# Performance work log

Measured on AMD Instinct MI355X. Metric: run time of the kernel, lower is better.

Reference implementation:

```python
import jax, jax.numpy as jnp
import numpy as np

N_NODES = 100000
N_EDGES = 1600000
HID = 128


def setup_inputs() -> dict:
    key = jax.random.key(0)
    ks = jax.random.split(key, 12)
    s = lambda fan_in: 1.0 / np.sqrt(fan_in)
    return {
        "x": jax.random.normal(ks[0], (N_NODES, HID), jnp.float32),
        "edge_index": jax.random.randint(ks[1], (2, N_EDGES), 0, N_NODES, jnp.int64),
        "edge_attr": jax.random.uniform(ks[2], (N_EDGES,), jnp.float32),
        "W_enc": jax.random.normal(ks[3], (HID, HID), jnp.float32) * s(HID),
        "b_enc": jax.random.normal(ks[4], (HID,), jnp.float32) * s(HID),
        "W_msg": jax.random.normal(ks[5], (HID + 1, HID), jnp.float32) * s(HID + 1),
        "b_msg": jax.random.normal(ks[6], (HID,), jnp.float32) * s(HID + 1),
        "W_upd": jax.random.normal(ks[7], (2 * HID, HID), jnp.float32) * s(2 * HID),
        "b_upd": jax.random.normal(ks[8], (HID,), jnp.float32) * s(2 * HID),
        "W_dec": jax.random.normal(ks[9], (HID, 1), jnp.float32) * s(HID),
        "b_dec": jax.random.normal(ks[10], (1,), jnp.float32) * s(HID),
    }


def reference(x, edge_index, edge_attr, W_enc, b_enc, W_msg, b_msg,
              W_upd, b_upd, W_dec, b_dec):
    n = x.shape[0]
    # encoder + relu
    h = jax.nn.relu(x @ W_enc + b_enc)                       # [N, H]
    src, dst = edge_index[0], edge_index[1]
    # message: gather x_j, concat scalar edge_attr, linear
    m = jnp.concatenate([h[src], edge_attr[:, None]], axis=-1) @ W_msg + b_msg  # [E, H]
    # scatter-min aggregate per destination node (nodes w/o in-edges -> 0, PyG convention)
    agg = jax.ops.segment_min(m, dst, num_segments=n)        # [N, H]
    agg = jnp.where(jnp.isinf(agg), jnp.zeros((), m.dtype), agg)
    # update: concat + linear
    u = jnp.concatenate([h, agg], axis=-1) @ W_upd + b_upd   # [N, H]
    # decoder + sigmoid
    return jax.nn.sigmoid(u @ W_dec + b_dec)                 # [N, 1]
```

## Files before the change

### kernel.cpp

```cpp
#include <hip/hip_runtime.h>

#define NN 100000
#define NE 1600000
#define HID 128
#define NBUCK 1563
#define CAP 1280
#define STP 130
#define SENT 3.0e38f
#define CH 8192
#define NCH 196
#define ENCB 391

typedef float f32x4 __attribute__((ext_vector_type(4)));
typedef __bf16 bf16x8 __attribute__((ext_vector_type(8)));
typedef unsigned short u16x8 __attribute__((ext_vector_type(8)));

static __device__ __forceinline__ unsigned short f2bf(float f) {
  union { float f; unsigned u; } v; v.f = f;
  unsigned u = v.u;
  return (unsigned short)((u + 0x7FFFu + ((u >> 16) & 1u)) >> 16);
}

static __device__ __forceinline__ f32x4 mfma_bf16(u16x8 a, u16x8 b, f32x4 c) {
  return __builtin_amdgcn_mfma_f32_16x16x32_bf16(
      __builtin_bit_cast(bf16x8, a), __builtin_bit_cast(bf16x8, b), c, 0, 0, 0);
}

static __device__ __forceinline__ int gidx(const int* __restrict__ ei, int is64, long long pos) {
  return is64 ? ei[pos * 2] : ei[pos];
}
static __device__ __forceinline__ int detect64(const int* __restrict__ ei, int tid) {
  unsigned long long bl = __ballot(ei[2 * (tid & 63) + 1] == 0);
  return (bl == ~0ull) ? 1 : 0;
}

__global__ __launch_bounds__(512) void k_prepw(const float* __restrict__ Wenc,
    const float* __restrict__ Wmsg, const float* __restrict__ Wupd,
    const float* __restrict__ Wdec, unsigned short* __restrict__ Wb,
    float* __restrict__ vprep, int* __restrict__ gcursor) {
  int b = blockIdx.x;
  int t = threadIdx.x;
  if (b == 96) {
    if (t < 128) {
      const float* row = Wupd + (size_t)(128 + t) * 128;
      float s = 0.f;
#pragma unroll 8
      for (int j = 0; j < 128; ++j) s = fmaf(row[j], Wdec[j], s);
      vprep[t] = s;
    }
    for (int i = t; i < NBUCK; i += 512) gcursor[i] = i * CAP;
    return;
  }
  int i = b * 512 + t;
  int m = i >> 14, idx = i & 16383;
  const float* src = (m == 0) ? Wenc : ((m == 1) ? Wmsg : Wupd);
  int k = idx >> 7, j = idx & 127;
  Wb[m * 17408 + j * 136 + k] = f2bf(src[idx]);
}

__global__ __launch_bounds__(512) void k_enc2(const float* __restrict__ x,
    const float* __restrict__ benc, const float* __restrict__ bupd,
    const float* __restrict__ Wdec, const unsigned short* __restrict__ Wb,
    unsigned* __restrict__ mNp, float* __restrict__ hdec) {
  __shared__ __align__(16) unsigned short Wt3[3 * 17408];
  __shared__ float bshE[128];
  __shared__ float bshU[128];
  __shared__ float wdsh[128];
  __shared__ unsigned short bounce[8][16 * 136];
  int tid = threadIdx.x;

  for (int i = tid; i < 6528; i += 512)
    ((uint4*)Wt3)[i] = ((const uint4*)Wb)[i];
  if (tid < 128) { bshE[tid] = benc[tid]; bshU[tid] = bupd[tid]; wdsh[tid] = Wdec[tid]; }
  __syncthreads();
  const unsigned short* WtE = Wt3;
  const unsigned short* WtM = Wt3 + 17408;
  const unsigned short* WtU = Wt3 + 2 * 17408;

  int wave = tid >> 6, lane = tid & 63;
  int l15 = lane & 15, lg = lane >> 4;
  f32x4 zero = {0.f, 0.f, 0.f, 0.f};

  for (int g = 0; g < 2; ++g) {
    int rowBase = blockIdx.x * 256 + g * 128 + wave * 16;
    int nodeA = rowBase + l15; if (nodeA > NN - 1) nodeA = NN - 1;

    u16x8 af[4];
#pragma unroll
    for (int kt = 0; kt < 4; ++kt) {
      const float* px = x + (long long)nodeA * HID + kt * 32 + lg * 8;
      f32x4 a0 = *(const f32x4*)px;
      f32x4 a1 = *(const f32x4*)(px + 4);
      u16x8 t;
      t[0] = f2bf(a0[0]); t[1] = f2bf(a0[1]); t[2] = f2bf(a0[2]); t[3] = f2bf(a0[3]);
      t[4] = f2bf(a1[0]); t[5] = f2bf(a1[1]); t[6] = f2bf(a1[2]); t[7] = f2bf(a1[3]);
      af[kt] = t;
    }
    f32x4 acc[8];
#pragma unroll
    for (int nt = 0; nt < 8; ++nt) acc[nt] = zero;
#pragma unroll
    for (int kt = 0; kt < 4; ++kt)
#pragma unroll
      for (int nt = 0; nt < 8; ++nt) {
        u16x8 bfv = *(const u16x8*)&WtE[(nt * 16 + l15) * 136 + kt * 32 + lg * 8];
        acc[nt] = mfma_bf16(af[kt], bfv, acc[nt]);
      }
#pragma unroll
    for (int nt = 0; nt < 8; ++nt) {
      int j = nt * 16 + l15;
      float bj = bshE[j];
#pragma unroll
      for (int r = 0; r < 4; ++r) {
        float v = acc[nt][r] + bj;
        v = v > 0.f ? v : 0.f;
        bounce[wave][(lg * 4 + r) * 136 + j] = f2bf(v);
      }
    }
    u16x8 ha[4];
#pragma unroll
    for (int kt = 0; kt < 4; ++kt)
      ha[kt] = *(const u16x8*)&bounce[wave][l15 * 136 + kt * 32 + lg * 8];
    asm volatile("s_waitcnt lgkmcnt(0)" ::: "memory");
    __builtin_amdgcn_sched_barrier(0);

    f32x4 acc2[8];
#pragma unroll
    for (int nt = 0; nt < 8; ++nt) acc2[nt] = zero;
#pragma unroll
    for (int kt = 0; kt < 4; ++kt)
#pragma unroll
      for (int nt = 0; nt < 8; ++nt) {
        u16x8 bfv = *(const u16x8*)&WtM[(nt * 16 + l15) * 136 + kt * 32 + lg * 8];
        acc2[nt] = mfma_bf16(ha[kt], bfv, acc2[nt]);
      }
#pragma unroll
    for (int nt = 0; nt < 8; ++nt) {
      int j = nt * 16 + l15;
#pragma unroll
      for (int r = 0; r < 4; ++r)
        bounce[wave][(lg * 4 + r) * 136 + j] = f2bf(acc2[nt][r]);
    }
    asm volatile("s_waitcnt lgkmcnt(0)" ::: "memory");
    __builtin_amdgcn_sched_barrier(0);
#pragma unroll 4
    for (int row = 0; row < 16; ++row) {
      int node = rowBase + row;
      if (node < NN) {
        unsigned lo = bounce[wave][row * 136 + lane];
        unsigned hi = bounce[wave][row * 136 + 64 + lane];
        mNp[(size_t)node * 64 + lane] = lo | (hi << 16);
      }
    }

    f32x4 acc3[8];
#pragma unroll
    for (int nt = 0; nt < 8; ++nt) acc3[nt] = zero;
#pragma unroll
    for (int kt = 0; kt < 4; ++kt)
#pragma unroll
      for (int nt = 0; nt < 8; ++nt) {
        u16x8 bfv = *(const u16x8*)&WtU[(nt * 16 + l15) * 136 + kt * 32 + lg * 8];
        acc3[nt] = mfma_bf16(ha[kt], bfv, acc3[nt]);
      }
    float hs0 = 0.f, hs1 = 0.f, hs2 = 0.f, hs3 = 0.f;
#pragma unroll
    for (int nt = 0; nt < 8; ++nt) {
      int j = nt * 16 + l15;
      float bu = bshU[j], wv = wdsh[j];
      hs0 += (acc3[nt][0] + bu) * wv;
      hs1 += (acc3[nt][1] + bu) * wv;
      hs2 += (acc3[nt][2] + bu) * wv;
      hs3 += (acc3[nt][3] + bu) * wv;
    }
#pragma unroll
    for (int m = 1; m < 16; m <<= 1) {
      hs0 += __shfl_xor(hs0, m);
      hs1 += __shfl_xor(hs1, m);
      hs2 += __shfl_xor(hs2, m);
      hs3 += __shfl_xor(hs3, m);
    }
    if (l15 == 0) {
      int n0 = rowBase + lg * 4;
      if (n0 + 3 < NN) {
        float4 st4; st4.x = hs0; st4.y = hs1; st4.z = hs2; st4.w = hs3;
        *(float4*)&hdec[n0] = st4;
      } else {
        if (n0 + 0 < NN) hdec[n0 + 0] = hs0;
        if (n0 + 1 < NN) hdec[n0 + 1] = hs1;
        if (n0 + 2 < NN) hdec[n0 + 2] = hs2;
        if (n0 + 3 < NN) hdec[n0 + 3] = hs3;
      }
    }
  }
}

__global__ __launch_bounds__(512) void k_sortscatter(const int* __restrict__ ei,
    const float* __restrict__ ea, int* __restrict__ gcursor,
    unsigned long long* __restrict__ csr) {
  __shared__ unsigned gbase[NBUCK];
  __shared__ unsigned cnt[NBUCK];
  int tid = threadIdx.x;
  int chunk = blockIdx.x;
  long long base = (long long)chunk * CH;
  int n = (int)(((long long)NE - base < CH) ? ((long long)NE - base) : CH);
  int is64 = detect64(ei, tid);
  for (int i = tid; i < NBUCK; i += 512) cnt[i] = 0;
  __syncthreads();
  for (int i = tid; i < n; i += 512) {
    int d = gidx(ei, is64, (long long)NE + base + i);
    atomicAdd(&cnt[d >> 6], 1u);
  }
  __syncthreads();
  for (int b = tid; b < NBUCK; b += 512) {
    unsigned c = cnt[b];
    gbase[b] = c ? (unsigned)atomicAdd(&gcursor[b], (int)c) : 0u;
  }
  __syncthreads();
  for (int i = tid; i < NBUCK; i += 512) cnt[i] = 0;
  __syncthreads();
  for (int i = tid; i < n; i += 512) {
    int s = gidx(ei, is64, base + i);
    int d = gidx(ei, is64, (long long)NE + base + i);
    unsigned eab = f2bf(ea[base + i]);
    int b = d >> 6;
    unsigned lp = atomicAdd(&cnt[b], 1u);
    unsigned lo = (unsigned)(s << 6) | ((unsigned)(d & 63) << 23);
    csr[gbase[b] + lp] = (unsigned long long)lo | ((unsigned long long)eab << 48);
  }
}

__global__ __launch_bounds__(512, 8) void k_msg(const unsigned* __restrict__ mNp,
    const float* __restrict__ Wmsg, const int* __restrict__ gcursor,
    const unsigned long long* __restrict__ csr, const float* __restrict__ bmsg,
    const float* __restrict__ vprep, const float* __restrict__ hdec,
    const float* __restrict__ bdec, float* __restrict__ out) {
  __shared__ float stf[64 * STP];
  int tid = threadIdx.x;
  int b = blockIdx.x;
  for (int i = tid; i < 64 * STP; i += 512) stf[i] = SENT;
  __syncthreads();

  int lane = tid & 63;
  int wv = tid >> 6;
  int off = b * CAP, end = gcursor[b];
  int cntE = end - off;
  int per = (cntE + 7) >> 3;
  int i0 = off + wv * per;
  int i1 = i0 + per; if (i1 > end) i1 = end;
  int iu = __builtin_amdgcn_readfirstlane(i0);
  int ie = __builtin_amdgcn_readfirstlane(i1);
  float wl0 = Wmsg[128 * 128 + lane];
  float wl1 = Wmsg[128 * 128 + 64 + lane];

#define EDGE_DO(PK, VV) do { \
    int loc_ = (int)(((unsigned)(PK) >> 23) & 0x3Fu); \
    float ea_ = __uint_as_float((unsigned)((PK) >> 32) & 0xFFFF0000u); \
    float a0_ = fmaf(ea_, wl0, __uint_as_float((VV) << 16)); \
    float a1_ = fmaf(ea_, wl1, __uint_as_float((VV) & 0xFFFF0000u)); \
    atomicMin(&stf[loc_ * STP + lane], a0_); \
    atomicMin(&stf[loc_ * STP + 64 + lane], a1_); \
  } while (0)

  int i = iu;
  for (; i + 16 <= ie; i += 16) {
    unsigned long long pk[16];
#pragma unroll
    for (int j = 0; j < 16; ++j) pk[j] = csr[i + j];
    unsigned v[16];
#pragma unroll
    for (int j = 0; j < 16; ++j)
      v[j] = mNp[((unsigned)pk[j] & 0x7FFFFFu) + lane];
#pragma unroll
    for (int j = 0; j < 16; ++j) EDGE_DO(pk[j], v[j]);
  }
  for (; i + 4 <= ie; i += 4) {
    unsigned long long pk[4];
#pragma unroll
    for (int j = 0; j < 4; ++j) pk[j] = csr[i + j];
    unsigned v[4];
#pragma unroll
    for (int j = 0; j < 4; ++j)
      v[j] = mNp[((unsigned)pk[j] & 0x7FFFFFu) + lane];
#pragma unroll
    for (int j = 0; j < 4; ++j) EDGE_DO(pk[j], v[j]);
  }
  for (; i < ie; ++i) {
    unsigned long long pk = csr[i];
    unsigned v = mNp[((unsigned)pk & 0x7FFFFFu) + lane];
    EDGE_DO(pk, v);
  }
#undef EDGE_DO
  __syncthreads();

  float vl0 = vprep[lane], vl1 = vprep[64 + lane];
  float bm0 = bmsg[lane], bm1 = bmsg[64 + lane];
  float bd = *bdec;
#pragma unroll
  for (int q = 0; q < 8; ++q) {
    int loc = (wv << 3) + q;
    float s0 = stf[loc * STP + lane];
    float s1 = stf[loc * STP + 64 + lane];
    float ps = ((s0 < 1.0e30f) ? (s0 + bm0) * vl0 : 0.f)
             + ((s1 < 1.0e30f) ? (s1 + bm1) * vl1 : 0.f);
#pragma unroll
    for (int m = 1; m < 64; m <<= 1) ps += __shfl_xor(ps, m);
    if (lane == 0) {
      int node = (b << 6) + loc;
      if (node < NN)
        out[node] = 1.f / (1.f + expf(-(ps + hdec[node] + bd)));
    }
  }
}

extern "C" void kernel_launch(void* const* d_in, const int* in_sizes, int n_in,
                              void* d_out, int out_size, void* d_ws, size_t ws_size,
                              hipStream_t stream) {
  const float* x    = (const float*)d_in[0];
  const int*   ei   = (const int*)d_in[1];
  const float* ea   = (const float*)d_in[2];
  const float* Wenc = (const float*)d_in[3];
  const float* benc = (const float*)d_in[4];
  const float* Wmsg = (const float*)d_in[5];
  const float* bmsg = (const float*)d_in[6];
  const float* Wupd = (const float*)d_in[7];
  const float* bupd = (const float*)d_in[8];
  const float* Wdec = (const float*)d_in[9];
  const float* bdec = (const float*)d_in[10];
  float* out = (float*)d_out;

  char* w = (char*)d_ws;
  auto alloc = [&](size_t bytes) { char* p = w; w += (bytes + 255) & ~(size_t)255; return p; };
  unsigned* mNp        = (unsigned*)alloc((size_t)NN * 64 * 4);
  unsigned long long* csr = (unsigned long long*)alloc((size_t)NBUCK * CAP * 8);
  unsigned short* Wb = (unsigned short*)alloc(3 * 17408 * 2);
  float* hdec   = (float*)alloc((size_t)NN * 4);
  float* vprep  = (float*)alloc(128 * 4);
  int* gcursor  = (int*)alloc((size_t)NBUCK * 4);

  k_prepw<<<97, 512, 0, stream>>>(Wenc, Wmsg, Wupd, Wdec, Wb, vprep, gcursor);
  k_enc2<<<ENCB, 512, 0, stream>>>(x, benc, bupd, Wdec, Wb, mNp, hdec);
  k_sortscatter<<<NCH, 512, 0, stream>>>(ei, ea, gcursor, csr);
  k_msg<<<NBUCK, 512, 0, stream>>>(mNp, Wmsg, gcursor, csr, bmsg, vprep, hdec, bdec, out);
}
```

Before: 132.5 us.

## Stage one weight matrix at a time in k_enc2 and cache dst indices in sortscatter

k_enc2 now holds a single 128x128 bf16 weight tile in LDS and reloads it three times (encoder, message, update), running the two row groups in phased passes. The encoded features are kept in registers between phases. This cuts LDS use from about 140KB to about 56KB per block so more blocks can be resident, and declares launch_bounds(512,4); in exchange it adds block-wide syncs and more register pressure. k_sortscatter doubles its chunk size (half as many blocks) and keeps each dst index in registers between the counting and scatter passes instead of reading it twice from global memory.

```diff
diff --git a/kernel.cpp b/kernel.cpp
--- a/kernel.cpp
+++ b/kernel.cpp
@@ -7,8 +7,8 @@
 #define CAP 1280
 #define STP 130
 #define SENT 3.0e38f
-#define CH 8192
-#define NCH 196
+#define CH 16384
+#define NCH 98
 #define ENCB 391
 
 typedef float f32x4 __attribute__((ext_vector_type(4)));
@@ -58,33 +58,30 @@
   Wb[m * 17408 + j * 136 + k] = f2bf(src[idx]);
 }
 
-__global__ __launch_bounds__(512) void k_enc2(const float* __restrict__ x,
+__global__ __launch_bounds__(512, 4) void k_enc2(const float* __restrict__ x,
     const float* __restrict__ benc, const float* __restrict__ bupd,
     const float* __restrict__ Wdec, const unsigned short* __restrict__ Wb,
     unsigned* __restrict__ mNp, float* __restrict__ hdec) {
-  __shared__ __align__(16) unsigned short Wt3[3 * 17408];
+  __shared__ __align__(16) unsigned short Wt[17408];
+  __shared__ unsigned short bounce[8][16 * 136];
   __shared__ float bshE[128];
   __shared__ float bshU[128];
   __shared__ float wdsh[128];
-  __shared__ unsigned short bounce[8][16 * 136];
   int tid = threadIdx.x;
-
-  for (int i = tid; i < 6528; i += 512)
-    ((uint4*)Wt3)[i] = ((const uint4*)Wb)[i];
   if (tid < 128) { bshE[tid] = benc[tid]; bshU[tid] = bupd[tid]; wdsh[tid] = Wdec[tid]; }
-  __syncthreads();
-  const unsigned short* WtE = Wt3;
-  const unsigned short* WtM = Wt3 + 17408;
-  const unsigned short* WtU = Wt3 + 2 * 17408;
 
   int wave = tid >> 6, lane = tid & 63;
   int l15 = lane & 15, lg = lane >> 4;
   f32x4 zero = {0.f, 0.f, 0.f, 0.f};
-
+  u16x8 haG[2][4];
+
+  for (int i = tid; i < 2176; i += 512)
+    ((uint4*)Wt)[i] = ((const uint4*)Wb)[i];
+  __syncthreads();
+#pragma unroll
   for (int g = 0; g < 2; ++g) {
     int rowBase = blockIdx.x * 256 + g * 128 + wave * 16;
     int nodeA = rowBase + l15; if (nodeA > NN - 1) nodeA = NN - 1;
-
     u16x8 af[4];
 #pragma unroll
     for (int kt = 0; kt < 4; ++kt) {
@@ -103,7 +100,7 @@
     for (int kt = 0; kt < 4; ++kt)
 #pragma unroll
       for (int nt = 0; nt < 8; ++nt) {
-        u16x8 bfv = *(const u16x8*)&WtE[(nt * 16 + l15) * 136 + kt * 32 + lg * 8];
+        u16x8 bfv = *(const u16x8*)&Wt[(nt * 16 + l15) * 136 + kt * 32 + lg * 8];
         acc[nt] = mfma_bf16(af[kt], bfv, acc[nt]);
       }
 #pragma unroll
@@ -117,13 +114,22 @@
         bounce[wave][(lg * 4 + r) * 136 + j] = f2bf(v);
       }
     }
-    u16x8 ha[4];
-#pragma unroll
-    for (int kt = 0; kt < 4; ++kt)
-      ha[kt] = *(const u16x8*)&bounce[wave][l15 * 136 + kt * 32 + lg * 8];
     asm volatile("s_waitcnt lgkmcnt(0)" ::: "memory");
     __builtin_amdgcn_sched_barrier(0);
-
+#pragma unroll
+    for (int kt = 0; kt < 4; ++kt)
+      haG[g][kt] = *(const u16x8*)&bounce[wave][l15 * 136 + kt * 32 + lg * 8];
+    asm volatile("s_waitcnt lgkmcnt(0)" ::: "memory");
+    __builtin_amdgcn_sched_barrier(0);
+  }
+  __syncthreads();
+
+  for (int i = tid; i < 2176; i += 512)
+    ((uint4*)Wt)[i] = ((const uint4*)Wb)[2176 + i];
+  __syncthreads();
+#pragma unroll
+  for (int g = 0; g < 2; ++g) {
+    int rowBase = blockIdx.x * 256 + g * 128 + wave * 16;
     f32x4 acc2[8];
 #pragma unroll
     for (int nt = 0; nt < 8; ++nt) acc2[nt] = zero;
@@ -131,8 +137,8 @@
     for (int kt = 0; kt < 4; ++kt)
 #pragma unroll
       for (int nt = 0; nt < 8; ++nt) {
-        u16x8 bfv = *(const u16x8*)&WtM[(nt * 16 + l15) * 136 + kt * 32 + lg * 8];
-        acc2[nt] = mfma_bf16(ha[kt], bfv, acc2[nt]);
+        u16x8 bfv = *(const u16x8*)&Wt[(nt * 16 + l15) * 136 + kt * 32 + lg * 8];
+        acc2[nt] = mfma_bf16(haG[g][kt], bfv, acc2[nt]);
       }
 #pragma unroll
     for (int nt = 0; nt < 8; ++nt) {
@@ -152,7 +158,17 @@
         mNp[(size_t)node * 64 + lane] = lo | (hi << 16);
       }
     }
-
+    asm volatile("s_waitcnt lgkmcnt(0)" ::: "memory");
+    __builtin_amdgcn_sched_barrier(0);
+  }
+  __syncthreads();
+
+  for (int i = tid; i < 2176; i += 512)
+    ((uint4*)Wt)[i] = ((const uint4*)Wb)[4352 + i];
+  __syncthreads();
+#pragma unroll
+  for (int g = 0; g < 2; ++g) {
+    int rowBase = blockIdx.x * 256 + g * 128 + wave * 16;
     f32x4 acc3[8];
 #pragma unroll
     for (int nt = 0; nt < 8; ++nt) acc3[nt] = zero;
@@ -160,8 +176,8 @@
     for (int kt = 0; kt < 4; ++kt)
 #pragma unroll
       for (int nt = 0; nt < 8; ++nt) {
-        u16x8 bfv = *(const u16x8*)&WtU[(nt * 16 + l15) * 136 + kt * 32 + lg * 8];
-        acc3[nt] = mfma_bf16(ha[kt], bfv, acc3[nt]);
+        u16x8 bfv = *(const u16x8*)&Wt[(nt * 16 + l15) * 136 + kt * 32 + lg * 8];
+        acc3[nt] = mfma_bf16(haG[g][kt], bfv, acc3[nt]);
       }
     float hs0 = 0.f, hs1 = 0.f, hs2 = 0.f, hs3 = 0.f;
 #pragma unroll
@@ -207,9 +223,15 @@
   int is64 = detect64(ei, tid);
   for (int i = tid; i < NBUCK; i += 512) cnt[i] = 0;
   __syncthreads();
-  for (int i = tid; i < n; i += 512) {
-    int d = gidx(ei, is64, (long long)NE + base + i);
-    atomicAdd(&cnt[d >> 6], 1u);
+  int dreg[CH / 512];
+#pragma unroll
+  for (int k = 0; k < CH / 512; ++k) {
+    int i = k * 512 + tid;
+    if (i < n) {
+      int d = gidx(ei, is64, (long long)NE + base + i);
+      dreg[k] = d;
+      atomicAdd(&cnt[d >> 6], 1u);
+    } else dreg[k] = -1;
   }
   __syncthreads();
   for (int b = tid; b < NBUCK; b += 512) {
@@ -219,14 +241,18 @@
   __syncthreads();
   for (int i = tid; i < NBUCK; i += 512) cnt[i] = 0;
   __syncthreads();
-  for (int i = tid; i < n; i += 512) {
-    int s = gidx(ei, is64, base + i);
-    int d = gidx(ei, is64, (long long)NE + base + i);
-    unsigned eab = f2bf(ea[base + i]);
-    int b = d >> 6;
-    unsigned lp = atomicAdd(&cnt[b], 1u);
-    unsigned lo = (unsigned)(s << 6) | ((unsigned)(d & 63) << 23);
-    csr[gbase[b] + lp] = (unsigned long long)lo | ((unsigned long long)eab << 48);
+#pragma unroll
+  for (int k = 0; k < CH / 512; ++k) {
+    int i = k * 512 + tid;
+    int d = dreg[k];
+    if (d >= 0) {
+      int s = gidx(ei, is64, base + i);
+      unsigned eab = f2bf(ea[base + i]);
+      int b = d >> 6;
+      unsigned lp = atomicAdd(&cnt[b], 1u);
+      unsigned lo = (unsigned)(s << 6) | ((unsigned)(d & 63) << 23);
+      csr[gbase[b] + lp] = (unsigned long long)lo | ((unsigned long long)eab << 48);
+    }
   }
 }
 
```

After: 136.0 us. 2.7% more time.
